# Kernel tuning notes

Hardware: AMD Instinct MI355X
Metric: run time of the kernel (lower is better)

The kernel has to match this reference:

```python
import jax, jax.numpy as jnp
import numpy as np

N, CS, CZ, CH, H, PQK, PV = 768, 384, 128, 16, 12, 4, 8
INF, EPS = 1e5, 1e-8


def setup_inputs() -> dict:
    key = jax.random.key(0)
    ks = jax.random.split(key, 12)
    w = lambda k, i, o: (jax.random.normal(k, (i, o), jnp.float32) * 0.02)
    inp = {
        's': jax.random.normal(ks[0], (N, CS), jnp.float32),
        'z': jax.random.normal(ks[1], (N, N, CZ), jnp.float32),
        'rot': jax.random.normal(ks[2], (N, 3, 3), jnp.float32),
        'trans': jax.random.normal(ks[3], (N, 3), jnp.float32),
        'mask': jnp.ones((N,), jnp.float32),
        'W_q': w(ks[4], CS, H * CH), 'b_q': jnp.zeros((H * CH,), jnp.float32),
        'W_kv': w(ks[5], CS, 2 * H * CH), 'b_kv': jnp.zeros((2 * H * CH,), jnp.float32),
        'W_qp': w(ks[6], CS, H * PQK * 3), 'b_qp': jnp.zeros((H * PQK * 3,), jnp.float32),
        'W_kvp': w(ks[7], CS, H * (PQK + PV) * 3), 'b_kvp': jnp.zeros((H * (PQK + PV) * 3,), jnp.float32),
        'W_b': w(ks[8], CZ, H), 'b_b': jnp.zeros((H,), jnp.float32),
        'head_weights': jnp.full((H,), 0.541324854612918, jnp.float32),  # softplus^-1(1)
        'W_out': w(ks[9], H * (CZ + CH + PV * 4), CS), 'b_out': jnp.zeros((CS,), jnp.float32),
    }
    return inp


def reference(s, z, rot, trans, mask, W_q, b_q, W_kv, b_kv, W_qp, b_qp, W_kvp, b_kvp,
              W_b, b_b, head_weights, W_out, b_out):
    n = s.shape[0]
    # scalar q/k/v
    q = (s @ W_q + b_q).reshape(n, H, CH)
    kv = (s @ W_kv + b_kv).reshape(n, H, 2 * CH)
    k, v = kv[..., :CH], kv[..., CH:]

    def make_points(W, b, P):
        p = (s @ W + b).reshape(n, 3, H * P)         # 3 contiguous coord chunks (x,y,z)
        p = jnp.transpose(p, (0, 2, 1))              # [n, H*P, 3]
        p = jnp.einsum('nij,npj->npi', rot, p) + trans[:, None, :]  # global frame
        return p.reshape(n, H, P, 3)

    q_pts = make_points(W_qp, b_qp, PQK)
    kv_pts = make_points(W_kvp, b_kvp, PQK + PV)
    k_pts, v_pts = kv_pts[:, :, :PQK], kv_pts[:, :, PQK:]

    b_pair = z @ W_b + b_b                                       # [n, n, H]
    a = jnp.einsum('qhc,khc->hqk', q, k) * np.sqrt(1.0 / (3 * CH))
    a = a + np.sqrt(1.0 / 3) * jnp.transpose(b_pair, (2, 0, 1))

    # point-distance attention term
    d2 = jnp.sum((q_pts[:, None] - k_pts[None]) ** 2, axis=-1)   # [q, k, H, Pqk]
    hw = jax.nn.softplus(head_weights) * np.sqrt(1.0 / (3 * (PQK * 9.0 / 2)))
    pt_att = -0.5 * jnp.sum(d2 * hw[None, None, :, None], axis=-1)  # [q, k, H]
    a = a + jnp.transpose(pt_att, (2, 0, 1))

    sq_mask = INF * (mask[:, None] * mask[None, :] - 1.0)
    a = jax.nn.softmax(a + sq_mask[None], axis=-1)               # [H, q, k]

    o = jnp.einsum('hqk,khc->qhc', a, v).reshape(n, H * CH)
    o_pt = jnp.einsum('hqk,khpc->qhpc', a, v_pts)                # [q, H, Pv, 3]
    o_pt = jnp.einsum('nba,nhpb->nhpa', rot, o_pt - trans[:, None, None, :])  # invert_apply
    o_pt_norm = jnp.sqrt(jnp.sum(o_pt ** 2, axis=-1) + EPS).reshape(n, H * PV)
    o_pt_flat = o_pt.reshape(n, H * PV, 3)
    o_pair = jnp.einsum('hqk,qkc->qhc', a, z).reshape(n, H * CZ)

    cat = jnp.concatenate([o, o_pt_flat[..., 0], o_pt_flat[..., 1], o_pt_flat[..., 2],
                           o_pt_norm, o_pair], axis=-1)          # [n, H*(CZ+CH+Pv*4)]
    return cat @ W_out + b_out
```

## Files before the change

kernel.cpp:

```cpp
#include <hip/hip_runtime.h>
#include <hip/hip_bf16.h>
#include <math.h>

#define NRES 768
#define CS   384
#define CZ   128
#define CH   16
#define NH   12
#define PQK  4
#define PV   8
#define QCOLS   (NH*CH)
#define KVCOLS  (2*NH*CH)
#define QPCOLS  (NH*PQK*3)
#define KVPCOLS (NH*(PQK+PV)*3)
#define CATC    (NH*(CZ+CH+PV*4))
#define NN      (NRES*NRES)

__global__ __launch_bounds__(256) void proj_kernel(
    const float* __restrict__ s,
    const float* __restrict__ Wq,  const float* __restrict__ bq,
    const float* __restrict__ Wkv, const float* __restrict__ bkv,
    const float* __restrict__ Wqp, const float* __restrict__ bqp,
    const float* __restrict__ Wkvp,const float* __restrict__ bkvp,
    float* __restrict__ proj_q, float* __restrict__ proj_kv,
    float* __restrict__ proj_qp, float* __restrict__ proj_kvp)
{
    __shared__ float Al[32][68];
    __shared__ float Bl[32][52];
    const int mt = blockIdx.x;
    const int gc0 = blockIdx.y * 48;
    const float* W; const float* bb; int ncol; float* dst; int c0;
    if (gc0 < 192)      { W=Wq;   bb=bq;   ncol=QCOLS;   dst=proj_q;   c0=gc0; }
    else if (gc0 < 576) { W=Wkv;  bb=bkv;  ncol=KVCOLS;  dst=proj_kv;  c0=gc0-192; }
    else if (gc0 < 720) { W=Wqp;  bb=bqp;  ncol=QPCOLS;  dst=proj_qp;  c0=gc0-576; }
    else                { W=Wkvp; bb=bkvp; ncol=KVPCOLS; dst=proj_kvp; c0=gc0-720; }
    const int tid = threadIdx.x;
    const int m0 = (tid & 15)*4;
    const int n0 = (tid >> 4)*3;
    float acc[4][3] = {};
    for (int kc = 0; kc < CS; kc += 32) {
        #pragma unroll
        for (int f = tid; f < 512; f += 256) {
            int r = f >> 3, c4 = (f & 7)*4;
            float4 v = *(const float4*)(s + (size_t)(mt*64+r)*CS + kc + c4);
            Al[c4][r]=v.x; Al[c4+1][r]=v.y; Al[c4+2][r]=v.z; Al[c4+3][r]=v.w;
        }
        for (int f = tid; f < 384; f += 256) {
            int r = f / 12, c4 = (f % 12)*4;
            *(float4*)&Bl[r][c4] = *(const float4*)(W + (size_t)(kc+r)*ncol + c0 + c4);
        }
        __syncthreads();
        #pragma unroll
        for (int kk = 0; kk < 32; ++kk) {
            float4 a = *(const float4*)&Al[kk][m0];
            float b0 = Bl[kk][n0], b1 = Bl[kk][n0+1], b2 = Bl[kk][n0+2];
            acc[0][0]+=a.x*b0; acc[0][1]+=a.x*b1; acc[0][2]+=a.x*b2;
            acc[1][0]+=a.y*b0; acc[1][1]+=a.y*b1; acc[1][2]+=a.y*b2;
            acc[2][0]+=a.z*b0; acc[2][1]+=a.z*b1; acc[2][2]+=a.z*b2;
            acc[3][0]+=a.w*b0; acc[3][1]+=a.w*b1; acc[3][2]+=a.w*b2;
        }
        __syncthreads();
    }
    #pragma unroll
    for (int r = 0; r < 4; ++r)
        #pragma unroll
        for (int c = 0; c < 3; ++c)
            dst[(size_t)(mt*64+m0+r)*ncol + c0+n0+c] = acc[r][c] + bb[c0+n0+c];
}

__global__ __launch_bounds__(256) void rotpts_kernel(
    const float* __restrict__ rot, const float* __restrict__ trans,
    const float* __restrict__ proj_q, const float* __restrict__ proj_kv,
    const float* __restrict__ proj_qp, const float* __restrict__ proj_kvp,
    const float* __restrict__ b_out,
    float* __restrict__ qfrag, float* __restrict__ kcat, float* __restrict__ vcatT,
    float* __restrict__ out)
{
    int g = blockIdx.x*256 + threadIdx.x;
    const int S0 = NRES*48;
    const int S1 = S0 + NRES*432;
    const int S2 = S1 + NRES*192;
    const int S3 = S2 + NRES*384;
    const int S4 = S3 + NRES*CS;
    if (g < S0) {
        int n = g/48, rem = g%48;
        int h = rem>>2, p = rem&3;
        float p0 = proj_qp[(size_t)n*QPCOLS + rem];
        float p1 = proj_qp[(size_t)n*QPCOLS + 48 + rem];
        float p2 = proj_qp[(size_t)n*QPCOLS + 96 + rem];
        const float* Rm = rot + (size_t)n*9; const float* t = trans + (size_t)n*3;
        float* dq = qfrag + ((size_t)n*12 + h)*28 + 16 + p*3;
        #pragma unroll
        for (int i = 0; i < 3; ++i)
            dq[i] = Rm[i*3]*p0 + Rm[i*3+1]*p1 + Rm[i*3+2]*p2 + t[i];
    } else if (g < S1) {
        int g2 = g - S0;
        int n = g2 % 768, t = g2 / 768;
        int h = t/36, u = t%36, p = u/3, i = u%3;
        int col = h*12 + p;
        float p0 = proj_kvp[(size_t)n*KVPCOLS + col];
        float p1 = proj_kvp[(size_t)n*KVPCOLS + 144 + col];
        float p2 = proj_kvp[(size_t)n*KVPCOLS + 288 + col];
        float val = rot[(size_t)n*9 + i*3]*p0 + rot[(size_t)n*9 + i*3+1]*p1
                  + rot[(size_t)n*9 + i*3+2]*p2 + trans[(size_t)n*3 + i];
        if (p < PQK) kcat[(size_t)(h*28 + 16 + p*3 + i)*NRES + n] = val;
        else         vcatT[(size_t)(h*40 + 16 + (p-4)*3 + i)*NRES + n] = val;
    } else if (g < S2) {
        int g3 = g - S1;
        int n = g3 / 192, c = g3 % 192;
        int h = c >> 4, cc = c & 15;
        qfrag[((size_t)n*12 + h)*28 + cc] = proj_q[(size_t)n*QCOLS + c];
    } else if (g < S3) {
        int g4 = g - S2;
        int n = g4 % 768, col = g4 / 768;
        int h = col >> 5, cc = col & 31;
        float val = proj_kv[(size_t)n*KVCOLS + col];
        if (cc < 16) kcat[(size_t)(h*28 + cc)*NRES + n] = val;
        else         vcatT[(size_t)(h*40 + (cc-16))*NRES + n] = val;
    } else if (g < S4) {
        int g5 = g - S3;
        out[g5] = b_out[g5 % CS];
    }
}

__global__ __launch_bounds__(256) void bias_kernel(
    const float* __restrict__ z, const float* __restrict__ mask,
    const float* __restrict__ W_b, const float* __restrict__ b_b,
    float* __restrict__ lg)
{
    int r = blockIdx.x*256 + threadIdx.x;
    int q = r / 768, k = r - q*768;
    const float4* zr = (const float4*)(z + (size_t)r*CZ);
    float acc[12] = {};
    #pragma unroll
    for (int c4 = 0; c4 < 32; ++c4) {
        float4 v = zr[c4];
        const float* w0 = W_b + c4*48;
        #pragma unroll
        for (int h = 0; h < 12; ++h)
            acc[h] += v.x*w0[h] + v.y*w0[12+h] + v.z*w0[24+h] + v.w*w0[36+h];
    }
    float mterm = 100000.0f*(mask[q]*mask[k] - 1.0f);
    const float scale_b = 0.5773502691896258f;
    #pragma unroll
    for (int h = 0; h < 12; ++h)
        lg[(size_t)h*NN + r] = scale_b*(acc[h] + b_b[h]) + mterm;
}

__global__ __launch_bounds__(256) void softmax_fused_kernel(
    float* __restrict__ lg, const float* __restrict__ qfrag, const float* __restrict__ kcat,
    const float* __restrict__ head_w, const float* __restrict__ vcatT,
    float* __restrict__ cat, float* __restrict__ optt)
{
    const int h = blockIdx.x % 12;
    const int q = (blockIdx.x / 12)*4 + (threadIdx.x >> 6);
    const int ln = threadIdx.x & 63;
    const float scale_qk = 0.14433756729740643f;
    float x = head_w[h];
    float sp = (x > 20.f) ? x : log1pf(__expf(x));
    float coef = -0.5f * sp * 0.13608276348795434f;

    float qf[28];
    const float* qp = qfrag + ((size_t)q*12 + h)*28;
    #pragma unroll
    for (int c = 0; c < 28; ++c) qf[c] = qp[c];

    float* arow = lg + (size_t)h*NN + (size_t)q*NRES;
    const float* kb = kcat + (size_t)h*28*NRES;
    float4 a[3];
    #pragma unroll
    for (int i = 0; i < 3; ++i) {
        a[i] = *(const float4*)(arow + ln*4 + i*256);
        float4 d = {0.f,0.f,0.f,0.f}, p2 = {0.f,0.f,0.f,0.f};
        #pragma unroll
        for (int c = 0; c < 16; ++c) {
            float4 kv = *(const float4*)(kb + (size_t)c*NRES + ln*4 + i*256);
            d.x += qf[c]*kv.x; d.y += qf[c]*kv.y; d.z += qf[c]*kv.z; d.w += qf[c]*kv.w;
        }
        #pragma unroll
        for (int c = 16; c < 28; ++c) {
            float4 kv = *(const float4*)(kb + (size_t)c*NRES + ln*4 + i*256);
            float t0 = qf[c]-kv.x, t1 = qf[c]-kv.y, t2 = qf[c]-kv.z, t3 = qf[c]-kv.w;
            p2.x += t0*t0; p2.y += t1*t1; p2.z += t2*t2; p2.w += t3*t3;
        }
        a[i].x += scale_qk*d.x + coef*p2.x;
        a[i].y += scale_qk*d.y + coef*p2.y;
        a[i].z += scale_qk*d.z + coef*p2.z;
        a[i].w += scale_qk*d.w + coef*p2.w;
    }
    float m = -1e30f;
    #pragma unroll
    for (int i=0;i<3;++i) m = fmaxf(m, fmaxf(fmaxf(a[i].x,a[i].y),fmaxf(a[i].z,a[i].w)));
    #pragma unroll
    for (int o=32;o>0;o>>=1) m = fmaxf(m, __shfl_xor(m,o,64));
    float ssum = 0.f;
    #pragma unroll
    for (int i=0;i<3;++i) {
        a[i].x = __expf(a[i].x-m); a[i].y = __expf(a[i].y-m);
        a[i].z = __expf(a[i].z-m); a[i].w = __expf(a[i].w-m);
        ssum += a[i].x + a[i].y + a[i].z + a[i].w;
    }
    #pragma unroll
    for (int o=32;o>0;o>>=1) ssum += __shfl_xor(ssum,o,64);
    float inv = 1.f/ssum;
    #pragma unroll
    for (int i=0;i<3;++i) {
        a[i].x*=inv; a[i].y*=inv; a[i].z*=inv; a[i].w*=inv;
        *(float4*)(arow + ln*4 + i*256) = a[i];
    }
    for (int col = 0; col < 40; ++col) {
        const float* vrow = vcatT + (size_t)(h*40+col)*NRES;
        float p = 0.f;
        #pragma unroll
        for (int i=0;i<3;++i) {
            float4 v = *(const float4*)(vrow + ln*4 + i*256);
            p += a[i].x*v.x + a[i].y*v.y + a[i].z*v.z + a[i].w*v.w;
        }
        #pragma unroll
        for (int o=32;o>0;o>>=1) p += __shfl_xor(p,o,64);
        if (ln == 0) {
            if (col < 16) cat[(size_t)q*CATC + h*16 + col] = p;
            else          optt[(size_t)q*288 + h*24 + (col-16)] = p;
        }
    }
}

__global__ __launch_bounds__(192) void opair_kernel(
    const float* __restrict__ z, const float* __restrict__ lg,
    const float* __restrict__ rot, const float* __restrict__ trans,
    const float* __restrict__ optt, float* __restrict__ cat)
{
    __shared__ float4 abuf4[2304];
    float* abuf = (float*)abuf4;
    const int q = blockIdx.x, tid = threadIdx.x;
    float* crow = cat + (size_t)q*CATC;

    for (int f = tid; f < 2304; f += 192) {
        int hh = f / 192, k4 = f % 192;
        abuf4[hh*192 + k4] = *(const float4*)(lg + (size_t)hh*NN + (size_t)q*NRES + k4*4);
    }
    __syncthreads();
    if (tid < 96) {
        int hh = tid>>3, p = tid&7;
        float b0 = optt[(size_t)q*288 + hh*24+p*3+0] - trans[q*3+0];
        float b1 = optt[(size_t)q*288 + hh*24+p*3+1] - trans[q*3+1];
        float b2 = optt[(size_t)q*288 + hh*24+p*3+2] - trans[q*3+2];
        const float* Rm = rot + (size_t)q*9;
        float v0 = Rm[0]*b0 + Rm[3]*b1 + Rm[6]*b2;
        float v1 = Rm[1]*b0 + Rm[4]*b1 + Rm[7]*b2;
        float v2 = Rm[2]*b0 + Rm[5]*b1 + Rm[8]*b2;
        crow[192 + tid] = v0;
        crow[288 + tid] = v1;
        crow[384 + tid] = v2;
        crow[480 + tid] = sqrtf(v0*v0 + v1*v1 + v2*v2 + 1e-8f);
    }
    const int h = tid >> 4, c8 = (tid & 15)*8;
    const float* zq = z + (size_t)q*NRES*CZ + c8;
    const float* ah = abuf + h*768;
    float4 acc0 = {0.f,0.f,0.f,0.f}, acc1 = {0.f,0.f,0.f,0.f};
    #pragma unroll 4
    for (int k = 0; k < NRES; ++k) {
        float aw = ah[k];
        float4 z0 = *(const float4*)(zq + (size_t)k*CZ);
        float4 z1 = *(const float4*)(zq + (size_t)k*CZ + 4);
        acc0.x += aw*z0.x; acc0.y += aw*z0.y; acc0.z += aw*z0.z; acc0.w += aw*z0.w;
        acc1.x += aw*z1.x; acc1.y += aw*z1.y; acc1.z += aw*z1.z; acc1.w += aw*z1.w;
    }
    *(float4*)(crow + 576 + h*128 + c8)     = acc0;
    *(float4*)(crow + 576 + h*128 + c8 + 4) = acc1;
}

__global__ __launch_bounds__(256) void outgemm_kernel(
    const float* __restrict__ cat, const float* __restrict__ W_out,
    float* __restrict__ out)
{
    __shared__ float Al[32][68];
    __shared__ float Bl[32][68];
    const int mt = blockIdx.x;
    const int nt = blockIdx.y;
    const int kt = blockIdx.z;
    const int tid = threadIdx.x;
    const int m0 = (tid & 15)*4, n0 = (tid >> 4)*4;
    float acc[4][4] = {};
    for (int ki = 0; ki < 11; ++ki) {
        int kc = kt*352 + ki*32;
        #pragma unroll
        for (int f = tid; f < 512; f += 256) {
            int r = f >> 3, c4 = (f & 7)*4;
            float4 v = *(const float4*)(cat + (size_t)(mt*64+r)*CATC + kc + c4);
            Al[c4][r]=v.x; Al[c4+1][r]=v.y; Al[c4+2][r]=v.z; Al[c4+3][r]=v.w;
        }
        #pragma unroll
        for (int f = tid; f < 512; f += 256) {
            int r = f >> 4, c4 = (f & 15)*4;
            *(float4*)&Bl[r][c4] = *(const float4*)(W_out + (size_t)(kc+r)*CS + nt*64 + c4);
        }
        __syncthreads();
        #pragma unroll
        for (int kk = 0; kk < 32; ++kk) {
            float4 a = *(const float4*)&Al[kk][m0];
            float4 b = *(const float4*)&Bl[kk][n0];
            acc[0][0]+=a.x*b.x; acc[0][1]+=a.x*b.y; acc[0][2]+=a.x*b.z; acc[0][3]+=a.x*b.w;
            acc[1][0]+=a.y*b.x; acc[1][1]+=a.y*b.y; acc[1][2]+=a.y*b.z; acc[1][3]+=a.y*b.w;
            acc[2][0]+=a.z*b.x; acc[2][1]+=a.z*b.y; acc[2][2]+=a.z*b.z; acc[2][3]+=a.z*b.w;
            acc[3][0]+=a.w*b.x; acc[3][1]+=a.w*b.y; acc[3][2]+=a.w*b.z; acc[3][3]+=a.w*b.w;
        }
        __syncthreads();
    }
    #pragma unroll
    for (int r = 0; r < 4; ++r)
        #pragma unroll
        for (int c = 0; c < 4; ++c)
            atomicAdd(&out[(size_t)(mt*64+m0+r)*CS + nt*64+n0+c], acc[r][c]);
}

extern "C" void kernel_launch(void* const* d_in, const int* in_sizes, int n_in,
                              void* d_out, int out_size, void* d_ws, size_t ws_size,
                              hipStream_t stream) {
    const float* s      = (const float*)d_in[0];
    const float* z      = (const float*)d_in[1];
    const float* rot    = (const float*)d_in[2];
    const float* trans  = (const float*)d_in[3];
    const float* mask   = (const float*)d_in[4];
    const float* W_q    = (const float*)d_in[5];
    const float* b_q    = (const float*)d_in[6];
    const float* W_kv   = (const float*)d_in[7];
    const float* b_kv   = (const float*)d_in[8];
    const float* W_qp   = (const float*)d_in[9];
    const float* b_qp   = (const float*)d_in[10];
    const float* W_kvp  = (const float*)d_in[11];
    const float* b_kvp  = (const float*)d_in[12];
    const float* W_b    = (const float*)d_in[13];
    const float* b_b    = (const float*)d_in[14];
    const float* head_w = (const float*)d_in[15];
    const float* W_out  = (const float*)d_in[16];
    const float* b_out  = (const float*)d_in[17];

    float* ws = (float*)d_ws;
    float* lg       = ws;
    float* proj_q   = ws;
    float* proj_kv  = ws + 147456;
    float* proj_qp  = ws + 442368;
    float* proj_kvp = ws + 552960;
    float* vcatT    = ws + 7077888;
    float* qfrag    = ws + 7446528;
    float* kcat     = ws + 7704576;
    float* optt     = ws + 7962624;
    float* cat      = ws + 8183808;
    float* out = (float*)d_out;

    proj_kernel<<<dim3(12,24), 256, 0, stream>>>(s, W_q, b_q, W_kv, b_kv, W_qp, b_qp, W_kvp, b_kvp,
                                                 proj_q, proj_kv, proj_qp, proj_kvp);
    rotpts_kernel<<<4320, 256, 0, stream>>>(rot, trans, proj_q, proj_kv, proj_qp, proj_kvp, b_out,
                                            qfrag, kcat, vcatT, out);
    bias_kernel<<<NN/256, 256, 0, stream>>>(z, mask, W_b, b_b, lg);
    softmax_fused_kernel<<<12*(NRES/4), 256, 0, stream>>>(lg, qfrag, kcat, head_w, vcatT, cat, optt);
    opair_kernel<<<NRES, 192, 0, stream>>>(z, lg, rot, trans, optt, cat);
    outgemm_kernel<<<dim3(12,6,6), 256, 0, stream>>>(cat, W_out, out);
}
```

Measured before the change: 801.9 us.

## Fuse pair bias, logits, softmax, value and pair aggregation into one per-query kernel

Replaces the bias, softmax and o_pair kernels with a single kernel that runs one 512-thread block per query row. Each block computes the pair bias, q·k and point-distance logits into a 36 KB shared-memory buffer, applies softmax there, then reduces values, points and z rows directly from shared memory. This removes the write and two re-reads of the full 12×N×N logit tensor in global memory. In exchange it reads the block's z row slab twice, gives up some parallelism in the logit phase, and the large shared allocation may limit occupancy.

```diff
diff --git a/kernel.cpp b/kernel.cpp
--- a/kernel.cpp
+++ b/kernel.cpp
@@ -123,128 +123,99 @@
     }
 }
 
-__global__ __launch_bounds__(256) void bias_kernel(
+__global__ __launch_bounds__(512, 6) void fused_attn_kernel(
     const float* __restrict__ z, const float* __restrict__ mask,
     const float* __restrict__ W_b, const float* __restrict__ b_b,
-    float* __restrict__ lg)
+    const float* __restrict__ qfrag, const float* __restrict__ kcat,
+    const float* __restrict__ head_w, const float* __restrict__ vcatT,
+    const float* __restrict__ rot, const float* __restrict__ trans,
+    float* __restrict__ cat)
 {
-    int r = blockIdx.x*256 + threadIdx.x;
-    int q = r / 768, k = r - q*768;
-    const float4* zr = (const float4*)(z + (size_t)r*CZ);
-    float acc[12] = {};
-    #pragma unroll
-    for (int c4 = 0; c4 < 32; ++c4) {
-        float4 v = zr[c4];
-        const float* w0 = W_b + c4*48;
-        #pragma unroll
-        for (int h = 0; h < 12; ++h)
-            acc[h] += v.x*w0[h] + v.y*w0[12+h] + v.z*w0[24+h] + v.w*w0[36+h];
-    }
-    float mterm = 100000.0f*(mask[q]*mask[k] - 1.0f);
-    const float scale_b = 0.5773502691896258f;
-    #pragma unroll
-    for (int h = 0; h < 12; ++h)
-        lg[(size_t)h*NN + r] = scale_b*(acc[h] + b_b[h]) + mterm;
-}
-
-__global__ __launch_bounds__(256) void softmax_fused_kernel(
-    float* __restrict__ lg, const float* __restrict__ qfrag, const float* __restrict__ kcat,
-    const float* __restrict__ head_w, const float* __restrict__ vcatT,
-    float* __restrict__ cat, float* __restrict__ optt)
-{
-    const int h = blockIdx.x % 12;
-    const int q = (blockIdx.x / 12)*4 + (threadIdx.x >> 6);
-    const int ln = threadIdx.x & 63;
+    __shared__ float lsm[12][768];
+    __shared__ float qf_l[12][28];
+    __shared__ float coef_l[12];
+    __shared__ float optl[12][24];
+    const int q = blockIdx.x;
+    const int tid = threadIdx.x;
+    for (int i = tid; i < 336; i += 512) qf_l[i/28][i - (i/28)*28] = qfrag[(size_t)q*336 + i];
+    if (tid < 12) {
+        float x = head_w[tid];
+        float sp = (x > 20.f) ? x : log1pf(__expf(x));
+        coef_l[tid] = -0.5f * sp * 0.13608276348795434f;
+    }
+    __syncthreads();
     const float scale_qk = 0.14433756729740643f;
-    float x = head_w[h];
-    float sp = (x > 20.f) ? x : log1pf(__expf(x));
-    float coef = -0.5f * sp * 0.13608276348795434f;
-
-    float qf[28];
-    const float* qp = qfrag + ((size_t)q*12 + h)*28;
-    #pragma unroll
-    for (int c = 0; c < 28; ++c) qf[c] = qp[c];
-
-    float* arow = lg + (size_t)h*NN + (size_t)q*NRES;
-    const float* kb = kcat + (size_t)h*28*NRES;
-    float4 a[3];
-    #pragma unroll
-    for (int i = 0; i < 3; ++i) {
-        a[i] = *(const float4*)(arow + ln*4 + i*256);
-        float4 d = {0.f,0.f,0.f,0.f}, p2 = {0.f,0.f,0.f,0.f};
-        #pragma unroll
-        for (int c = 0; c < 16; ++c) {
-            float4 kv = *(const float4*)(kb + (size_t)c*NRES + ln*4 + i*256);
-            d.x += qf[c]*kv.x; d.y += qf[c]*kv.y; d.z += qf[c]*kv.z; d.w += qf[c]*kv.w;
-        }
-        #pragma unroll
-        for (int c = 16; c < 28; ++c) {
-            float4 kv = *(const float4*)(kb + (size_t)c*NRES + ln*4 + i*256);
-            float t0 = qf[c]-kv.x, t1 = qf[c]-kv.y, t2 = qf[c]-kv.z, t3 = qf[c]-kv.w;
-            p2.x += t0*t0; p2.y += t1*t1; p2.z += t2*t2; p2.w += t3*t3;
-        }
-        a[i].x += scale_qk*d.x + coef*p2.x;
-        a[i].y += scale_qk*d.y + coef*p2.y;
-        a[i].z += scale_qk*d.z + coef*p2.z;
-        a[i].w += scale_qk*d.w + coef*p2.w;
-    }
-    float m = -1e30f;
-    #pragma unroll
-    for (int i=0;i<3;++i) m = fmaxf(m, fmaxf(fmaxf(a[i].x,a[i].y),fmaxf(a[i].z,a[i].w)));
-    #pragma unroll
-    for (int o=32;o>0;o>>=1) m = fmaxf(m, __shfl_xor(m,o,64));
-    float ssum = 0.f;
-    #pragma unroll
-    for (int i=0;i<3;++i) {
-        a[i].x = __expf(a[i].x-m); a[i].y = __expf(a[i].y-m);
-        a[i].z = __expf(a[i].z-m); a[i].w = __expf(a[i].w-m);
-        ssum += a[i].x + a[i].y + a[i].z + a[i].w;
-    }
-    #pragma unroll
-    for (int o=32;o>0;o>>=1) ssum += __shfl_xor(ssum,o,64);
-    float inv = 1.f/ssum;
-    #pragma unroll
-    for (int i=0;i<3;++i) {
-        a[i].x*=inv; a[i].y*=inv; a[i].z*=inv; a[i].w*=inv;
-        *(float4*)(arow + ln*4 + i*256) = a[i];
-    }
-    for (int col = 0; col < 40; ++col) {
+    const float scale_b  = 0.5773502691896258f;
+    const float mq = mask[q];
+
+    for (int k = tid; k < NRES; k += 512) {
+        const float4* zr = (const float4*)(z + ((size_t)q*NRES + k)*CZ);
+        float bacc[12] = {};
+        #pragma unroll
+        for (int c4 = 0; c4 < 32; ++c4) {
+            float4 v = zr[c4];
+            const float* w0 = W_b + c4*48;
+            #pragma unroll
+            for (int h = 0; h < 12; ++h)
+                bacc[h] += v.x*w0[h] + v.y*w0[12+h] + v.z*w0[24+h] + v.w*w0[36+h];
+        }
+        const float mterm = 100000.0f*(mq*mask[k] - 1.0f);
+        #pragma unroll
+        for (int h = 0; h < 12; ++h) {
+            const float* kb = kcat + ((size_t)(h*28))*NRES + k;
+            float d = 0.f;
+            #pragma unroll
+            for (int c = 0; c < 16; ++c) d += qf_l[h][c]*kb[(size_t)c*NRES];
+            float p2 = 0.f;
+            #pragma unroll
+            for (int c = 16; c < 28; ++c) { float t = qf_l[h][c] - kb[(size_t)c*NRES]; p2 += t*t; }
+            lsm[h][k] = scale_qk*d + coef_l[h]*p2 + scale_b*(bacc[h] + b_b[h]) + mterm;
+        }
+    }
+    __syncthreads();
+
+    const int w = tid >> 6, ln = tid & 63;
+    for (int h = w; h < 12; h += 8) {
+        float* row = lsm[h];
+        float vv[12]; float mx = -1e30f;
+        #pragma unroll
+        for (int j = 0; j < 12; ++j) { vv[j] = row[ln + j*64]; mx = fmaxf(mx, vv[j]); }
+        #pragma unroll
+        for (int o = 32; o > 0; o >>= 1) mx = fmaxf(mx, __shfl_xor(mx, o, 64));
+        float s = 0.f;
+        #pragma unroll
+        for (int j = 0; j < 12; ++j) { vv[j] = __expf(vv[j]-mx); s += vv[j]; }
+        #pragma unroll
+        for (int o = 32; o > 0; o >>= 1) s += __shfl_xor(s, o, 64);
+        float inv = 1.f/s;
+        #pragma unroll
+        for (int j = 0; j < 12; ++j) row[ln + j*64] = vv[j]*inv;
+    }
+    __syncthreads();
+
+    float* crow = cat + (size_t)q*CATC;
+
+    for (int r = w; r < 480; r += 8) {
+        const int h = r/40, col = r - (r/40)*40;
         const float* vrow = vcatT + (size_t)(h*40+col)*NRES;
+        const float* ar = lsm[h];
         float p = 0.f;
         #pragma unroll
-        for (int i=0;i<3;++i) {
-            float4 v = *(const float4*)(vrow + ln*4 + i*256);
-            p += a[i].x*v.x + a[i].y*v.y + a[i].z*v.z + a[i].w*v.w;
-        }
-        #pragma unroll
-        for (int o=32;o>0;o>>=1) p += __shfl_xor(p,o,64);
+        for (int j = 0; j < 12; ++j) p += ar[ln + j*64]*vrow[ln + j*64];
+        #pragma unroll
+        for (int o = 32; o > 0; o >>= 1) p += __shfl_xor(p, o, 64);
         if (ln == 0) {
-            if (col < 16) cat[(size_t)q*CATC + h*16 + col] = p;
-            else          optt[(size_t)q*288 + h*24 + (col-16)] = p;
-        }
-    }
-}
-
-__global__ __launch_bounds__(192) void opair_kernel(
-    const float* __restrict__ z, const float* __restrict__ lg,
-    const float* __restrict__ rot, const float* __restrict__ trans,
-    const float* __restrict__ optt, float* __restrict__ cat)
-{
-    __shared__ float4 abuf4[2304];
-    float* abuf = (float*)abuf4;
-    const int q = blockIdx.x, tid = threadIdx.x;
-    float* crow = cat + (size_t)q*CATC;
-
-    for (int f = tid; f < 2304; f += 192) {
-        int hh = f / 192, k4 = f % 192;
-        abuf4[hh*192 + k4] = *(const float4*)(lg + (size_t)hh*NN + (size_t)q*NRES + k4*4);
+            if (col < 16) crow[h*16 + col] = p;
+            else          optl[h][col-16] = p;
+        }
     }
     __syncthreads();
+
     if (tid < 96) {
-        int hh = tid>>3, p = tid&7;
-        float b0 = optt[(size_t)q*288 + hh*24+p*3+0] - trans[q*3+0];
-        float b1 = optt[(size_t)q*288 + hh*24+p*3+1] - trans[q*3+1];
-        float b2 = optt[(size_t)q*288 + hh*24+p*3+2] - trans[q*3+2];
+        const int hh = tid >> 3, p = tid & 7;
+        float b0 = optl[hh][p*3+0] - trans[q*3+0];
+        float b1 = optl[hh][p*3+1] - trans[q*3+1];
+        float b2 = optl[hh][p*3+2] - trans[q*3+2];
         const float* Rm = rot + (size_t)q*9;
         float v0 = Rm[0]*b0 + Rm[3]*b1 + Rm[6]*b2;
         float v1 = Rm[1]*b0 + Rm[4]*b1 + Rm[7]*b2;
@@ -254,20 +225,25 @@
         crow[384 + tid] = v2;
         crow[480 + tid] = sqrtf(v0*v0 + v1*v1 + v2*v2 + 1e-8f);
     }
-    const int h = tid >> 4, c8 = (tid & 15)*8;
-    const float* zq = z + (size_t)q*NRES*CZ + c8;
-    const float* ah = abuf + h*768;
-    float4 acc0 = {0.f,0.f,0.f,0.f}, acc1 = {0.f,0.f,0.f,0.f};
-    #pragma unroll 4
-    for (int k = 0; k < NRES; ++k) {
-        float aw = ah[k];
-        float4 z0 = *(const float4*)(zq + (size_t)k*CZ);
-        float4 z1 = *(const float4*)(zq + (size_t)k*CZ + 4);
-        acc0.x += aw*z0.x; acc0.y += aw*z0.y; acc0.z += aw*z0.z; acc0.w += aw*z0.w;
-        acc1.x += aw*z1.x; acc1.y += aw*z1.y; acc1.z += aw*z1.z; acc1.w += aw*z1.w;
-    }
-    *(float4*)(crow + 576 + h*128 + c8)     = acc0;
-    *(float4*)(crow + 576 + h*128 + c8 + 4) = acc1;
+
+    if (tid < 384) {
+        const int h = tid >> 5, c4 = tid & 31;
+        const float* zq = z + (size_t)q*NRES*CZ + c4*4;
+        const float* ah = lsm[h];
+        float4 acc = {0.f,0.f,0.f,0.f};
+        for (int k = 0; k < NRES; k += 4) {
+            float4 a4 = *(const float4*)(ah + k);
+            float4 z0 = *(const float4*)(zq + (size_t)(k+0)*CZ);
+            float4 z1 = *(const float4*)(zq + (size_t)(k+1)*CZ);
+            float4 z2 = *(const float4*)(zq + (size_t)(k+2)*CZ);
+            float4 z3 = *(const float4*)(zq + (size_t)(k+3)*CZ);
+            acc.x += a4.x*z0.x + a4.y*z1.x + a4.z*z2.x + a4.w*z3.x;
+            acc.y += a4.x*z0.y + a4.y*z1.y + a4.z*z2.y + a4.w*z3.y;
+            acc.z += a4.x*z0.z + a4.y*z1.z + a4.z*z2.z + a4.w*z3.z;
+            acc.w += a4.x*z0.w + a4.y*z1.w + a4.z*z2.w + a4.w*z3.w;
+        }
+        *(float4*)(crow + 576 + h*128 + c4*4) = acc;
+    }
 }
 
 __global__ __launch_bounds__(256) void outgemm_kernel(
@@ -337,24 +313,21 @@
     const float* b_out  = (const float*)d_in[17];
 
     float* ws = (float*)d_ws;
-    float* lg       = ws;
     float* proj_q   = ws;
     float* proj_kv  = ws + 147456;
     float* proj_qp  = ws + 442368;
     float* proj_kvp = ws + 552960;
-    float* vcatT    = ws + 7077888;
-    float* qfrag    = ws + 7446528;
-    float* kcat     = ws + 7704576;
-    float* optt     = ws + 7962624;
-    float* cat      = ws + 8183808;
+    float* qfrag    = ws + 884736;
+    float* kcat     = ws + 1142784;
+    float* vcatT    = ws + 1400832;
+    float* cat      = ws + 1769472;
     float* out = (float*)d_out;
 
     proj_kernel<<<dim3(12,24), 256, 0, stream>>>(s, W_q, b_q, W_kv, b_kv, W_qp, b_qp, W_kvp, b_kvp,
                                                  proj_q, proj_kv, proj_qp, proj_kvp);
     rotpts_kernel<<<4320, 256, 0, stream>>>(rot, trans, proj_q, proj_kv, proj_qp, proj_kvp, b_out,
                                             qfrag, kcat, vcatT, out);
-    bias_kernel<<<NN/256, 256, 0, stream>>>(z, mask, W_b, b_b, lg);
-    softmax_fused_kernel<<<12*(NRES/4), 256, 0, stream>>>(lg, qfrag, kcat, head_w, vcatT, cat, optt);
-    opair_kernel<<<NRES, 192, 0, stream>>>(z, lg, rot, trans, optt, cat);
+    fused_attn_kernel<<<NRES, 512, 0, stream>>>(z, mask, W_b, b_b, qfrag, kcat, head_w, vcatT,
+                                                rot, trans, cat);
     outgemm_kernel<<<dim3(12,6,6), 256, 0, stream>>>(cat, W_out, out);
 }
```

After: 1.170 ms. 45.8% more time.

## Restructure opair kernel so each thread accumulates all heads, reusing z loads

Applied to the files above, without the earlier changes.

The pair-output kernel now assigns each thread 4 channels across all 12 heads over a 96-wide slice of k. Each z element is therefore loaded once per block instead of once per head. Partial sums from the 8 k-groups are reduced through a shared-memory buffer with serialized synchronized stages. This cuts redundant z reads, at the cost of more registers, extra shared memory and reduction barriers.

```diff
diff --git a/kernel.cpp b/kernel.cpp
--- a/kernel.cpp
+++ b/kernel.cpp
@@ -225,21 +225,23 @@
     }
 }
 
-__global__ __launch_bounds__(192) void opair_kernel(
+__global__ __launch_bounds__(256, 2) void opair_kernel(
     const float* __restrict__ z, const float* __restrict__ lg,
     const float* __restrict__ rot, const float* __restrict__ trans,
     const float* __restrict__ optt, float* __restrict__ cat)
 {
-    __shared__ float4 abuf4[2304];
-    float* abuf = (float*)abuf4;
+    __shared__ float abuf[12][768];
+    __shared__ float obuf[12][132];
     const int q = blockIdx.x, tid = threadIdx.x;
     float* crow = cat + (size_t)q*CATC;
 
-    for (int f = tid; f < 2304; f += 192) {
+    for (int f = tid; f < 2304; f += 256) {
         int hh = f / 192, k4 = f % 192;
-        abuf4[hh*192 + k4] = *(const float4*)(lg + (size_t)hh*NN + (size_t)q*NRES + k4*4);
-    }
+        *(float4*)&abuf[hh][k4*4] = *(const float4*)(lg + (size_t)hh*NN + (size_t)q*NRES + (size_t)k4*4);
+    }
+    for (int f = tid; f < 12*132; f += 256) ((float*)obuf)[f] = 0.f;
     __syncthreads();
+
     if (tid < 96) {
         int hh = tid>>3, p = tid&7;
         float b0 = optt[(size_t)q*288 + hh*24+p*3+0] - trans[q*3+0];
@@ -254,20 +256,40 @@
         crow[384 + tid] = v2;
         crow[480 + tid] = sqrtf(v0*v0 + v1*v1 + v2*v2 + 1e-8f);
     }
-    const int h = tid >> 4, c8 = (tid & 15)*8;
-    const float* zq = z + (size_t)q*NRES*CZ + c8;
-    const float* ah = abuf + h*768;
-    float4 acc0 = {0.f,0.f,0.f,0.f}, acc1 = {0.f,0.f,0.f,0.f};
+
+    const int c4 = (tid & 31)*4;
+    const int kg = tid >> 5;
+    const float* zq = z + (size_t)q*NRES*CZ + c4;
+    float4 acc[12];
+    #pragma unroll
+    for (int h = 0; h < 12; ++h) acc[h] = make_float4(0.f,0.f,0.f,0.f);
+    const int k0 = kg*96;
     #pragma unroll 4
-    for (int k = 0; k < NRES; ++k) {
-        float aw = ah[k];
-        float4 z0 = *(const float4*)(zq + (size_t)k*CZ);
-        float4 z1 = *(const float4*)(zq + (size_t)k*CZ + 4);
-        acc0.x += aw*z0.x; acc0.y += aw*z0.y; acc0.z += aw*z0.z; acc0.w += aw*z0.w;
-        acc1.x += aw*z1.x; acc1.y += aw*z1.y; acc1.z += aw*z1.z; acc1.w += aw*z1.w;
-    }
-    *(float4*)(crow + 576 + h*128 + c8)     = acc0;
-    *(float4*)(crow + 576 + h*128 + c8 + 4) = acc1;
+    for (int k = k0; k < k0+96; ++k) {
+        float4 zv = *(const float4*)(zq + (size_t)k*CZ);
+        #pragma unroll
+        for (int h = 0; h < 12; ++h) {
+            float aw = abuf[h][k];
+            acc[h].x += aw*zv.x; acc[h].y += aw*zv.y;
+            acc[h].z += aw*zv.z; acc[h].w += aw*zv.w;
+        }
+    }
+    for (int g = 0; g < 8; ++g) {
+        __syncthreads();
+        if (kg == g) {
+            #pragma unroll
+            for (int h = 0; h < 12; ++h) {
+                obuf[h][c4+0] += acc[h].x; obuf[h][c4+1] += acc[h].y;
+                obuf[h][c4+2] += acc[h].z; obuf[h][c4+3] += acc[h].w;
+            }
+        }
+    }
+    __syncthreads();
+    for (int f = tid; f < 384; f += 256) {
+        int h = f >> 5, cc4 = (f & 31)*4;
+        float4 o = *(const float4*)&obuf[h][cc4];
+        *(float4*)(crow + 576 + h*128 + cc4) = o;
+    }
 }
 
 __global__ __launch_bounds__(256) void outgemm_kernel(
@@ -355,6 +377,6 @@
                                             qfrag, kcat, vcatT, out);
     bias_kernel<<<NN/256, 256, 0, stream>>>(z, mask, W_b, b_b, lg);
     softmax_fused_kernel<<<12*(NRES/4), 256, 0, stream>>>(lg, qfrag, kcat, head_w, vcatT, cat, optt);
-    opair_kernel<<<NRES, 192, 0, stream>>>(z, lg, rot, trans, optt, cat);
+    opair_kernel<<<NRES, 256, 0, stream>>>(z, lg, rot, trans, optt, cat);
     outgemm_kernel<<<dim3(12,6,6), 256, 0, stream>>>(cat, W_out, out);
 }
```

New measurement: 727.9 us (median of 2 runs). 9.2% less time.
